# Kernel optimization log

Hardware: AMD Instinct MI355X
Metric: run time of the kernel (lower is better)

Reference implementation:

```python
import jax, jax.numpy as jnp
import numpy as np

B, S, D, H, L, OUT = 4, 1024, 1024, 16, 6, 512
HD = D // H
EPS = 1e-5


def _positional_encoding(seq, dim):
    pos = np.arange(seq, dtype=np.float32)[:, None]          # [S,1]
    i = np.arange(0, dim, 2, dtype=np.float32)[None, :]       # even indices
    div = np.power(10000.0, 2.0 * i / dim)                    # repo's (nonstandard) exponent
    pe = np.zeros((seq, dim), dtype=np.float32)
    pe[:, 0::2] = np.sin(pos / div)
    pe[:, 1::2] = np.cos(pos / div)
    return jnp.asarray(pe)[None]                               # [1,S,D]


def _causal_mask(seq):
    r = jnp.arange(seq)
    m = jnp.where(r[None, :] > r[:, None], jnp.float32(-jnp.inf), jnp.float32(0.0))
    return m[None, None]                                       # [1,1,S,S]


def setup_inputs() -> dict:
    key = jax.random.key(0)
    ks = jax.random.split(key, 10)
    sc = 0.02
    inp = {
        'x':      jax.random.normal(ks[0], (B, S, D), jnp.float32),
        'pe':     _positional_encoding(S, D),
        'mask':   _causal_mask(S),
        'ln1_g':  jnp.ones((L, D), jnp.float32),
        'ln1_b':  jnp.zeros((L, D), jnp.float32),
        'wq':     jax.random.normal(ks[1], (L, D, D), jnp.float32) * sc,
        'wk':     jax.random.normal(ks[2], (L, D, D), jnp.float32) * sc,
        'wv':     jax.random.normal(ks[3], (L, D, D), jnp.float32) * sc,
        'wo':     jax.random.normal(ks[4], (L, D, D), jnp.float32) * sc,
        'ln2_g':  jnp.ones((L, D), jnp.float32),
        'ln2_b':  jnp.zeros((L, D), jnp.float32),
        'wf':     jax.random.normal(ks[5], (L, D, D), jnp.float32) * sc,
        'lnf_g':  jnp.ones((D,), jnp.float32),
        'lnf_b':  jnp.zeros((D,), jnp.float32),
        'w_out':  jax.random.normal(ks[6], (OUT, D), jnp.float32) * sc,
    }
    return inp


def _layer_norm(x, g, b):
    mu = jnp.mean(x, axis=-1, keepdims=True)
    var = jnp.mean(jnp.square(x - mu), axis=-1, keepdims=True)
    return (x - mu) * jax.lax.rsqrt(var + EPS) * g + b


def _split_heads(x):
    b, s, d = x.shape
    return x.reshape(b, s, H, HD).transpose(0, 2, 1, 3)  # [B,H,S,HD]


def reference(x, pe, mask, ln1_g, ln1_b, wq, wk, wv, wo, ln2_g, ln2_b, wf, lnf_g, lnf_b, w_out):
    h = x + pe
    scale = 1.0 / jnp.sqrt(jnp.float32(HD))
    for l in range(wq.shape[0]):
        h_ = _layer_norm(h, ln1_g[l], ln1_b[l])
        q = _split_heads(jnp.einsum('bsd,ed->bse', h_, wq[l]))
        k = _split_heads(jnp.einsum('bsd,ed->bse', h_, wk[l]))
        v = _split_heads(jnp.einsum('bsd,ed->bse', h_, wv[l]))
        scores = jnp.einsum('bhqd,bhkd->bhqk', q, k) * scale + mask  # [B,H,S,S]
        probs = jax.nn.softmax(scores, axis=-1)
        attn = jnp.einsum('bhqk,bhkd->bhqd', probs, v)
        attn = attn.transpose(0, 2, 1, 3).reshape(h.shape)            # combine heads
        h = h + jnp.einsum('bsd,ed->bse', attn, wo[l])
        h_ = _layer_norm(h, ln2_g[l], ln2_b[l])
        h = h + jnp.einsum('bsd,ed->bse', h_, wf[l])                  # FFN = plain linear (no activation, as in source)
    h = _layer_norm(h, lnf_g, lnf_b)
    return jnp.einsum('bsd,od->bso', h, w_out)
```

## Files before the change

kernel.cpp:

```cpp
#include <hip/hip_runtime.h>
#include <hip/hip_bf16.h>
#include <stdint.h>

#define BATCH 4
#define SEQ   1024
#define DIM   1024
#define NH    16
#define HDIM  64
#define NLAYER 6
#define NOUT  512
#define NTOK  (BATCH*SEQ)
#define LOG2E 1.44269504088896f
#define NEG_BIG (-1e30f)
#define VTS   72

using bf16 = __hip_bfloat16;
typedef __attribute__((ext_vector_type(4))) float f32x4;
typedef __attribute__((ext_vector_type(8))) short bf16x8;

typedef __attribute__((address_space(1))) void as1_void;
typedef __attribute__((address_space(3))) void as3_void;

__device__ __forceinline__ float bf2f(short u) {
  union { unsigned int i; float f; } c;
  c.i = ((unsigned int)(unsigned short)u) << 16;
  return c.f;
}

__device__ __forceinline__ short f2bs(float f) {
  bf16 h = __float2bfloat16(f);
  return *(short*)&h;
}

__device__ __forceinline__ float exp_clamped(float x) {
  return exp2f(fmaxf(x, -100.f) * LOG2E);
}

__device__ __forceinline__ float loadf(const void* p, size_t i, bool f32) {
  return f32 ? ((const float*)p)[i] : __bfloat162float(((const bf16*)p)[i]);
}

__device__ __forceinline__ void g2l16(const void* g, void* l) {
  __builtin_amdgcn_global_load_lds((const as1_void*)g, (as3_void*)l, 16, 0, 0);
}

__global__ void sniff(const unsigned int* __restrict__ w, int* __restrict__ flag) {
  const int lane = threadIdx.x;
  const unsigned int word = w[lane];
  const int e2 = (word >> 7) & 0xFF;
  const bool bf16ish = (e2 >= 0x60) && (e2 <= 0x8F);
  const unsigned long long m = __ballot(bf16ish);
  if (lane == 0) *flag = (__popcll(m) >= 48) ? 0 : 1;
}

#define CV_BIG 786432
#define CV_TOT (5 * CV_BIG + 65536)

__global__ __launch_bounds__(256) void convert_all(
    const float* __restrict__ s0, const float* __restrict__ s1,
    const float* __restrict__ s2, const float* __restrict__ s3,
    const float* __restrict__ s4, const float* __restrict__ s5,
    bf16* __restrict__ d0, bf16* __restrict__ d1, bf16* __restrict__ d2,
    bf16* __restrict__ d3, bf16* __restrict__ d4, bf16* __restrict__ d5,
    const int* __restrict__ flag) {
  if (*flag == 0) return;
  for (size_t vi = (size_t)blockIdx.x * 256 + threadIdx.x; vi < CV_TOT;
       vi += (size_t)gridDim.x * 256) {
    const int t = (int)(vi / CV_BIG);
    const float* s; bf16* d;
    switch (t) {
      case 0: s = s0; d = d0; break;
      case 1: s = s1; d = d1; break;
      case 2: s = s2; d = d2; break;
      case 3: s = s3; d = d3; break;
      case 4: s = s4; d = d4; break;
      default: s = s5; d = d5; break;
    }
    const size_t off = (vi - (size_t)t * CV_BIG) * 8;
    const f32x4 a = *(const f32x4*)(s + off);
    const f32x4 b = *(const f32x4*)(s + off + 4);
    bf16x8 o;
    o[0] = f2bs(a[0]); o[1] = f2bs(a[1]); o[2] = f2bs(a[2]); o[3] = f2bs(a[3]);
    o[4] = f2bs(b[0]); o[5] = f2bs(b[1]); o[6] = f2bs(b[2]); o[7] = f2bs(b[3]);
    *(bf16x8*)(d + off) = o;
  }
}

template<int EPI>
__device__ __forceinline__ void gemm_body(const bf16* __restrict__ A,
                                          const bf16* __restrict__ W,
                                          void* __restrict__ C,
                                          const int* __restrict__ flag,
                                          int N, int m0, int n0) {
  __shared__ __align__(16) bf16 lA[128 * 32];
  __shared__ __align__(16) bf16 lB[128 * 32];
  const int tid  = threadIdx.x;
  const int wave = tid >> 6;
  const int lane = tid & 63;
  const int quad = lane >> 4;
  const int l16  = lane & 15;
  const int wm = (wave >> 1) * 64;
  const int wn = (wave & 1) * 64;
  const int K = DIM;

  const int r0 = tid >> 2;
  const int c0 = (tid & 3) * 8;
  const int r1 = (tid + 256) >> 2;

  bool f32out = false;
  if (EPI == 2) f32out = (*flag != 0);

  f32x4 acc[4][4];
#pragma unroll
  for (int i = 0; i < 4; ++i)
#pragma unroll
    for (int j = 0; j < 4; ++j) acc[i][j] = (f32x4){0.f, 0.f, 0.f, 0.f};

  for (int k0 = 0; k0 < K; k0 += 32) {
    __syncthreads();
    g2l16(A + (size_t)(m0 + r0) * K + k0 + c0, lA + 512 * wave);
    g2l16(A + (size_t)(m0 + r1) * K + k0 + c0, lA + 2048 + 512 * wave);
    g2l16(W + (size_t)(n0 + r0) * K + k0 + c0, lB + 512 * wave);
    g2l16(W + (size_t)(n0 + r1) * K + k0 + c0, lB + 2048 + 512 * wave);
    __builtin_amdgcn_s_waitcnt(0);
    __syncthreads();

    bf16x8 af[4], bfr[4];
#pragma unroll
    for (int i = 0; i < 4; ++i) {
      af[i]  = *(const bf16x8*)(lA + (wm + i * 16 + l16) * 32 + quad * 8);
      bfr[i] = *(const bf16x8*)(lB + (wn + i * 16 + l16) * 32 + quad * 8);
    }
#pragma unroll
    for (int i = 0; i < 4; ++i)
#pragma unroll
      for (int j = 0; j < 4; ++j)
        acc[i][j] = __builtin_amdgcn_mfma_f32_16x16x32_bf16(af[i], bfr[j], acc[i][j], 0, 0, 0);
  }

#pragma unroll
  for (int i = 0; i < 4; ++i) {
    const int rowb = m0 + wm + i * 16 + quad * 4;
#pragma unroll
    for (int j = 0; j < 4; ++j) {
      const int col = n0 + wn + j * 16 + l16;
#pragma unroll
      for (int r = 0; r < 4; ++r) {
        const size_t idx = (size_t)(rowb + r) * N + col;
        const float v = acc[i][j][r];
        if (EPI == 0) ((bf16*)C)[idx] = __float2bfloat16(v);
        else { if (f32out) ((float*)C)[idx] = v; else ((bf16*)C)[idx] = __float2bfloat16(v); }
      }
    }
  }
}

__global__ __launch_bounds__(256) void gemm_out(const bf16* __restrict__ A,
                                                const bf16* __restrict__ Wc,
                                                const bf16* __restrict__ Wo,
                                                void* __restrict__ C,
                                                const int* __restrict__ flag) {
  const bf16* W = (*flag != 0) ? Wc : Wo;
  gemm_body<2>(A, W, C, flag, NOUT, blockIdx.y * 128, blockIdx.x * 128);
}

__global__ __launch_bounds__(256) void gemm_qkv(const bf16* __restrict__ A,
                                                const bf16* __restrict__ cq,
                                                const bf16* __restrict__ ck,
                                                const bf16* __restrict__ cvv,
                                                const bf16* __restrict__ oq,
                                                const bf16* __restrict__ ok,
                                                const bf16* __restrict__ ov,
                                                bf16* __restrict__ q,
                                                bf16* __restrict__ k,
                                                bf16* __restrict__ v,
                                                const int* __restrict__ flag) {
  const int gx = blockIdx.x;
  const int sel = gx >> 3;
  const int n0 = (gx & 7) * 128;
  const bool f32 = (*flag != 0);
  const bf16* W = (sel == 0) ? (f32 ? cq : oq)
                 : (sel == 1) ? (f32 ? ck : ok)
                              : (f32 ? cvv : ov);
  bf16* C = (sel == 0) ? q : (sel == 1 ? k : v);
  gemm_body<0>(A, W, C, nullptr, DIM, blockIdx.y * 128, n0);
}

__device__ __forceinline__ void gemm64_body(const bf16* __restrict__ A,
                                            const bf16* __restrict__ W,
                                            float* __restrict__ C,
                                            int N, int m0, int n0) {
  __shared__ __align__(16) bf16 lA[64 * 32];
  __shared__ __align__(16) bf16 lB[128 * 32];
  const int tid  = threadIdx.x;
  const int wave = tid >> 6;
  const int lane = tid & 63;
  const int quad = lane >> 4;
  const int l16  = lane & 15;
  const int wm = (wave >> 1) * 32;
  const int wn = (wave & 1) * 64;
  const int K = DIM;

  const int r0 = tid >> 2;
  const int c0 = (tid & 3) * 8;
  const int r1 = (tid + 256) >> 2;

  f32x4 acc[2][4];
#pragma unroll
  for (int i = 0; i < 2; ++i)
#pragma unroll
    for (int j = 0; j < 4; ++j) acc[i][j] = (f32x4){0.f, 0.f, 0.f, 0.f};

  for (int k0 = 0; k0 < K; k0 += 32) {
    __syncthreads();
    g2l16(A + (size_t)(m0 + r0) * K + k0 + c0, lA + 512 * wave);
    g2l16(W + (size_t)(n0 + r0) * K + k0 + c0, lB + 512 * wave);
    g2l16(W + (size_t)(n0 + r1) * K + k0 + c0, lB + 2048 + 512 * wave);
    __builtin_amdgcn_s_waitcnt(0);
    __syncthreads();

    bf16x8 af[2], bfr[4];
#pragma unroll
    for (int i = 0; i < 2; ++i)
      af[i]  = *(const bf16x8*)(lA + (wm + i * 16 + l16) * 32 + quad * 8);
#pragma unroll
    for (int j = 0; j < 4; ++j)
      bfr[j] = *(const bf16x8*)(lB + (wn + j * 16 + l16) * 32 + quad * 8);
#pragma unroll
    for (int i = 0; i < 2; ++i)
#pragma unroll
      for (int j = 0; j < 4; ++j)
        acc[i][j] = __builtin_amdgcn_mfma_f32_16x16x32_bf16(af[i], bfr[j], acc[i][j], 0, 0, 0);
  }

#pragma unroll
  for (int i = 0; i < 2; ++i) {
    const int rowb = m0 + wm + i * 16 + quad * 4;
#pragma unroll
    for (int j = 0; j < 4; ++j) {
      const int col = n0 + wn + j * 16 + l16;
#pragma unroll
      for (int r = 0; r < 4; ++r)
        C[(size_t)(rowb + r) * N + col] += acc[i][j][r];
    }
  }
}

__global__ __launch_bounds__(256) void gemm_add(const bf16* __restrict__ A,
                                                const bf16* __restrict__ Wc,
                                                const bf16* __restrict__ Wo,
                                                const int* __restrict__ flag,
                                                float* __restrict__ C) {
  const bf16* W = (*flag != 0) ? Wc : Wo;
  gemm64_body(A, W, C, DIM, blockIdx.y * 64, blockIdx.x * 128);
}

__global__ __launch_bounds__(256) void add_pe(const void* __restrict__ x,
                                              const void* __restrict__ pe,
                                              float* __restrict__ h,
                                              const int* __restrict__ flag) {
  const bool f32 = (*flag != 0);
  const size_t i = (size_t)blockIdx.x * 256 + threadIdx.x;
  h[i] = loadf(x, i, f32) + loadf(pe, i & (SEQ * DIM - 1), f32);
}

__global__ __launch_bounds__(256) void layernorm(const float* __restrict__ x,
                                                 const void* __restrict__ g,
                                                 const void* __restrict__ b,
                                                 int loff,
                                                 bf16* __restrict__ y,
                                                 const int* __restrict__ flag) {
  const bool f32 = (*flag != 0);
  const int row = blockIdx.x;
  const int tid = threadIdx.x;
  const int wave = tid >> 6;
  const float* xr = x + (size_t)row * DIM;
  __shared__ float red[8];

  float v[4];
  float s = 0.f;
#pragma unroll
  for (int i = 0; i < 4; ++i) { v[i] = xr[tid + 256 * i]; s += v[i]; }
#pragma unroll
  for (int off = 32; off >= 1; off >>= 1) s += __shfl_xor(s, off);
  if ((tid & 63) == 0) red[wave] = s;
  __syncthreads();
  const float mu = (red[0] + red[1] + red[2] + red[3]) * (1.f / DIM);

  float vs = 0.f;
#pragma unroll
  for (int i = 0; i < 4; ++i) { const float d = v[i] - mu; vs += d * d; }
#pragma unroll
  for (int off = 32; off >= 1; off >>= 1) vs += __shfl_xor(vs, off);
  if ((tid & 63) == 0) red[4 + wave] = vs;
  __syncthreads();
  const float var = (red[4] + red[5] + red[6] + red[7]) * (1.f / DIM);
  const float rs = rsqrtf(var + 1e-5f);

#pragma unroll
  for (int i = 0; i < 4; ++i) {
    const int d = tid + 256 * i;
    const float gv = loadf(g, (size_t)loff + d, f32);
    const float bv = loadf(b, (size_t)loff + d, f32);
    y[(size_t)row * DIM + d] = __float2bfloat16((v[i] - mu) * rs * gv + bv);
  }
}

__global__ __launch_bounds__(256, 2) void attn_flash(const bf16* __restrict__ q,
                                                     const bf16* __restrict__ k,
                                                     const bf16* __restrict__ v,
                                                     bf16* __restrict__ o) {
  __shared__ __align__(16) short lK[64 * 64];
  __shared__ __align__(16) short lVT[64 * VTS];
  __shared__ __align__(16) short lP[4 * 16 * VTS];

  const int idx = blockIdx.x;
  const int qt = (SEQ / 64 - 1) - (idx >> 6);
  const int bh = idx & 63;
  const int hh = bh & (NH - 1);
  const int bb = bh >> 4;
  const int q0 = qt * 64;

  const int tid = threadIdx.x;
  const int wave = tid >> 6;
  const int lane = tid & 63;
  const int quad = lane >> 4;
  const int l16 = lane & 15;

  const size_t base = (size_t)bb * SEQ * DIM + hh * HDIM;
  const int qlo = q0 + wave * 16;

  bf16x8 qf[2];
  {
    const bf16* qr = q + base + (size_t)(qlo + l16) * DIM;
#pragma unroll
    for (int kc = 0; kc < 2; ++kc) {
      bf16x8 t = *(const bf16x8*)(qr + kc * 32 + quad * 8);
      bf16x8 sq;
#pragma unroll
      for (int e = 0; e < 8; ++e) sq[e] = f2bs(bf2f(t[e]) * 0.125f);
      qf[kc] = sq;
    }
  }

  float l_acc[4] = {0.f, 0.f, 0.f, 0.f};
  f32x4 oacc[4];
#pragma unroll
  for (int nb = 0; nb < 4; ++nb) oacc[nb] = (f32x4){0.f, 0.f, 0.f, 0.f};

  short* lPw = lP + wave * 16 * VTS;
  const int nt = qt + 1;

  for (int t = 0; t < nt; ++t) {
    const int kbase = t * 64;
    __syncthreads();

    {
      const int r8 = lane >> 3;
      const int cc = (lane & 7) ^ r8;
#pragma unroll
      for (int c = 0; c < 2; ++c) {
        const int row = wave * 16 + c * 8 + r8;
        g2l16(k + base + (size_t)(kbase + row) * DIM + cc * 8,
              lK + (wave * 16 + c * 8) * 64);
      }
    }

    bf16x8 vch[2];
#pragma unroll
    for (int c2 = 0; c2 < 2; ++c2) {
      const int cid = tid + c2 * 256;
      const int kk = cid >> 3;
      const int d0 = (cid & 7) * 8;
      vch[c2] = *(const bf16x8*)(v + base + (size_t)(kbase + kk) * DIM + d0);
    }
#pragma unroll
    for (int c2 = 0; c2 < 2; ++c2) {
      const int cid = tid + c2 * 256;
      const int kk = cid >> 3;
      const int d0 = (cid & 7) * 8;
#pragma unroll
      for (int e = 0; e < 8; ++e) {
        const int d = d0 + e;
        const int kks = kk ^ (((d >> 3) & 7) << 3);
        lVT[d * VTS + kks] = vch[c2][e];
      }
    }
    __builtin_amdgcn_s_waitcnt(0);
    __syncthreads();

    f32x4 s[4];
#pragma unroll
    for (int nb = 0; nb < 4; ++nb) {
      f32x4 acc = (f32x4){0.f, 0.f, 0.f, 0.f};
      const int n = nb * 16 + l16;
#pragma unroll
      for (int kc = 0; kc < 2; ++kc) {
        const int cidx = (kc * 4 + quad) ^ (n & 7);
        bf16x8 kf = *(const bf16x8*)(lK + n * 64 + cidx * 8);
        acc = __builtin_amdgcn_mfma_f32_16x16x32_bf16(qf[kc], kf, acc, 0, 0, 0);
      }
      s[nb] = acc;
    }

    if (kbase + 63 > qlo) {
#pragma unroll
      for (int nb = 0; nb < 4; ++nb) {
        const int j = kbase + nb * 16 + l16;
#pragma unroll
        for (int r = 0; r < 4; ++r)
          if (j > qlo + quad * 4 + r) s[nb][r] = NEG_BIG;
      }
    }

#pragma unroll
    for (int nb = 0; nb < 4; ++nb) {
#pragma unroll
      for (int r = 0; r < 4; ++r) {
        const float p = exp_clamped(s[nb][r]);
        l_acc[r] += p;
        lPw[(quad * 4 + r) * VTS + nb * 16 + l16] = f2bs(p);
      }
    }

    __builtin_amdgcn_s_waitcnt(0);
    bf16x8 pf[2];
#pragma unroll
    for (int kc = 0; kc < 2; ++kc)
      pf[kc] = *(const bf16x8*)(lPw + l16 * VTS + kc * 32 + quad * 8);

#pragma unroll
    for (int nb = 0; nb < 4; ++nb) {
      const int n = nb * 16 + l16;
      const int swz = ((n >> 3) & 7) << 3;
#pragma unroll
      for (int kc = 0; kc < 2; ++kc) {
        const int kchunk = (kc * 32 + quad * 8) ^ swz;
        bf16x8 vf = *(const bf16x8*)(lVT + n * VTS + kchunk);
        oacc[nb] = __builtin_amdgcn_mfma_f32_16x16x32_bf16(pf[kc], vf, oacc[nb], 0, 0, 0);
      }
    }
  }

  float linv[4];
#pragma unroll
  for (int r = 0; r < 4; ++r) {
    float ts = l_acc[r];
#pragma unroll
    for (int off = 8; off >= 1; off >>= 1) ts += __shfl_xor(ts, off);
    linv[r] = 1.f / ts;
  }
#pragma unroll
  for (int nb = 0; nb < 4; ++nb)
#pragma unroll
    for (int r = 0; r < 4; ++r) {
      const int qrow = q0 + wave * 16 + quad * 4 + r;
      o[base + (size_t)qrow * DIM + nb * 16 + l16] =
          __float2bfloat16(oacc[nb][r] * linv[r]);
    }
}

extern "C" void kernel_launch(void* const* d_in, const int* in_sizes, int n_in,
                              void* d_out, int out_size, void* d_ws, size_t ws_size,
                              hipStream_t stream) {
  const void* x    = d_in[0];
  const void* pe   = d_in[1];
  const void* ln1g = d_in[3];
  const void* ln1b = d_in[4];
  const void* wq   = d_in[5];
  const void* wk   = d_in[6];
  const void* wv   = d_in[7];
  const void* wo   = d_in[8];
  const void* ln2g = d_in[9];
  const void* ln2b = d_in[10];
  const void* wf   = d_in[11];
  const void* lnfg = d_in[12];
  const void* lnfb = d_in[13];
  const void* wout = d_in[14];

  const size_t MB = 1u << 20;
  char* ws = (char*)d_ws;
  int*  flag = (int*)ws;
  bf16* wqc  = (bf16*)(ws + 1 * MB);
  bf16* wkc  = (bf16*)(ws + 13 * MB);
  bf16* wvc  = (bf16*)(ws + 25 * MB);
  bf16* woc  = (bf16*)(ws + 37 * MB);
  bf16* wfc  = (bf16*)(ws + 49 * MB);
  bf16* woutc= (bf16*)(ws + 61 * MB);
  float* h   = (float*)(ws + 62 * MB);
  bf16* hn   = (bf16*)(ws + 78 * MB);
  bf16* qb   = (bf16*)(ws + 86 * MB);
  bf16* kb   = (bf16*)(ws + 94 * MB);
  bf16* vb   = (bf16*)(ws + 102 * MB);
  bf16* ab   = hn;

  sniff<<<1, 64, 0, stream>>>((const unsigned int*)wq, flag);

  convert_all<<<2048, 256, 0, stream>>>(
      (const float*)wq, (const float*)wk, (const float*)wv,
      (const float*)wo, (const float*)wf, (const float*)wout,
      wqc, wkc, wvc, woc, wfc, woutc, flag);

  add_pe<<<NTOK * DIM / 256, 256, 0, stream>>>(x, pe, h, flag);

  for (int l = 0; l < NLAYER; ++l) {
    const size_t woff = (size_t)l << 20;
    const int poff = l * DIM;
    layernorm<<<NTOK, 256, 0, stream>>>(h, ln1g, ln1b, poff, hn, flag);
    gemm_qkv<<<dim3(24, 32), 256, 0, stream>>>(
        hn, wqc + woff, wkc + woff, wvc + woff,
        (const bf16*)wq + woff, (const bf16*)wk + woff, (const bf16*)wv + woff,
        qb, kb, vb, flag);
    attn_flash<<<dim3(BATCH * NH * (SEQ / 64)), 256, 0, stream>>>(qb, kb, vb, ab);
    gemm_add<<<dim3(8, 64), 256, 0, stream>>>(ab, woc + woff,
                                              (const bf16*)wo + woff, flag, h);
    layernorm<<<NTOK, 256, 0, stream>>>(h, ln2g, ln2b, poff, hn, flag);
    gemm_add<<<dim3(8, 64), 256, 0, stream>>>(hn, wfc + woff,
                                              (const bf16*)wf + woff, flag, h);
  }

  layernorm<<<NTOK, 256, 0, stream>>>(h, lnfg, lnfb, 0, hn, flag);
  gemm_out<<<dim3(4, 32), 256, 0, stream>>>(hn, woutc, (const bf16*)wout,
                                            d_out, flag);
}
```

Before: 966.4 us.

## Remap GEMM and attention block IDs for XCD-aware L2 locality; restructure weight conversion

Block indices for the QKV, projection, output GEMMs and flash attention are remapped so that blocks dispatched round-robin across the 8 XCDs (obid & 7) handle contiguous tiles. Tiles sharing weight columns or the same batch-head then land on one XCD and can reuse its L2. The weight conversion kernel also drops its grid-stride loop with a division for a fixed block-to-tensor mapping, with four vector loads per thread to raise memory-level parallelism. The cost is hardcoded grid sizes tied to the exact problem dimensions.

```diff
diff --git a/kernel.cpp b/kernel.cpp
--- a/kernel.cpp
+++ b/kernel.cpp
@@ -53,9 +53,6 @@
   if (lane == 0) *flag = (__popcll(m) >= 48) ? 0 : 1;
 }
 
-#define CV_BIG 786432
-#define CV_TOT (5 * CV_BIG + 65536)
-
 __global__ __launch_bounds__(256) void convert_all(
     const float* __restrict__ s0, const float* __restrict__ s1,
     const float* __restrict__ s2, const float* __restrict__ s3,
@@ -64,25 +61,27 @@
     bf16* __restrict__ d3, bf16* __restrict__ d4, bf16* __restrict__ d5,
     const int* __restrict__ flag) {
   if (*flag == 0) return;
-  for (size_t vi = (size_t)blockIdx.x * 256 + threadIdx.x; vi < CV_TOT;
-       vi += (size_t)gridDim.x * 256) {
-    const int t = (int)(vi / CV_BIG);
-    const float* s; bf16* d;
-    switch (t) {
-      case 0: s = s0; d = d0; break;
-      case 1: s = s1; d = d1; break;
-      case 2: s = s2; d = d2; break;
-      case 3: s = s3; d = d3; break;
-      case 4: s = s4; d = d4; break;
-      default: s = s5; d = d5; break;
-    }
-    const size_t off = (vi - (size_t)t * CV_BIG) * 8;
-    const f32x4 a = *(const f32x4*)(s + off);
-    const f32x4 b = *(const f32x4*)(s + off + 4);
+  int b = blockIdx.x;
+  const float* s; bf16* d;
+  if      (b <  768) { s = s0; d = d0; }
+  else if (b < 1536) { s = s1; d = d1; b -= 768; }
+  else if (b < 2304) { s = s2; d = d2; b -= 1536; }
+  else if (b < 3072) { s = s3; d = d3; b -= 2304; }
+  else if (b < 3840) { s = s4; d = d4; b -= 3072; }
+  else               { s = s5; d = d5; b -= 3840; }
+  const size_t e0 = ((size_t)b * 1024 + threadIdx.x) * 8;
+  f32x4 a[4], c[4];
+#pragma unroll
+  for (int i = 0; i < 4; ++i) {
+    a[i] = *(const f32x4*)(s + e0 + i * 2048);
+    c[i] = *(const f32x4*)(s + e0 + i * 2048 + 4);
+  }
+#pragma unroll
+  for (int i = 0; i < 4; ++i) {
     bf16x8 o;
-    o[0] = f2bs(a[0]); o[1] = f2bs(a[1]); o[2] = f2bs(a[2]); o[3] = f2bs(a[3]);
-    o[4] = f2bs(b[0]); o[5] = f2bs(b[1]); o[6] = f2bs(b[2]); o[7] = f2bs(b[3]);
-    *(bf16x8*)(d + off) = o;
+    o[0] = f2bs(a[i][0]); o[1] = f2bs(a[i][1]); o[2] = f2bs(a[i][2]); o[3] = f2bs(a[i][3]);
+    o[4] = f2bs(c[i][0]); o[5] = f2bs(c[i][1]); o[6] = f2bs(c[i][2]); o[7] = f2bs(c[i][3]);
+    *(bf16x8*)(d + e0 + i * 2048) = o;
   }
 }
 
@@ -160,8 +159,12 @@
                                                 const bf16* __restrict__ Wo,
                                                 void* __restrict__ C,
                                                 const int* __restrict__ flag) {
+  const int obid = blockIdx.x;
+  const int wid = (obid & 7) * 16 + (obid >> 3);
+  const int m0 = (wid & 31) * 128;
+  const int n0 = (wid >> 5) * 128;
   const bf16* W = (*flag != 0) ? Wc : Wo;
-  gemm_body<2>(A, W, C, flag, NOUT, blockIdx.y * 128, blockIdx.x * 128);
+  gemm_body<2>(A, W, C, flag, NOUT, m0, n0);
 }
 
 __global__ __launch_bounds__(256) void gemm_qkv(const bf16* __restrict__ A,
@@ -175,15 +178,18 @@
                                                 bf16* __restrict__ k,
                                                 bf16* __restrict__ v,
                                                 const int* __restrict__ flag) {
-  const int gx = blockIdx.x;
-  const int sel = gx >> 3;
-  const int n0 = (gx & 7) * 128;
+  const int obid = blockIdx.x;
+  const int wid = (obid & 7) * 96 + (obid >> 3);
+  const int m0   = (wid & 31) * 128;
+  const int rest = wid >> 5;
+  const int sel  = rest >> 3;
+  const int n0   = (rest & 7) * 128;
   const bool f32 = (*flag != 0);
   const bf16* W = (sel == 0) ? (f32 ? cq : oq)
                  : (sel == 1) ? (f32 ? ck : ok)
                               : (f32 ? cvv : ov);
   bf16* C = (sel == 0) ? q : (sel == 1 ? k : v);
-  gemm_body<0>(A, W, C, nullptr, DIM, blockIdx.y * 128, n0);
+  gemm_body<0>(A, W, C, nullptr, DIM, m0, n0);
 }
 
 __device__ __forceinline__ void gemm64_body(const bf16* __restrict__ A,
@@ -251,8 +257,12 @@
                                                 const bf16* __restrict__ Wo,
                                                 const int* __restrict__ flag,
                                                 float* __restrict__ C) {
+  const int obid = blockIdx.x;
+  const int wid = (obid & 7) * 64 + (obid >> 3);
+  const int m0 = (wid & 63) * 64;
+  const int n0 = (wid >> 6) * 128;
   const bf16* W = (*flag != 0) ? Wc : Wo;
-  gemm64_body(A, W, C, DIM, blockIdx.y * 64, blockIdx.x * 128);
+  gemm64_body(A, W, C, DIM, m0, n0);
 }
 
 __global__ __launch_bounds__(256) void add_pe(const void* __restrict__ x,
@@ -314,9 +324,10 @@
   __shared__ __align__(16) short lVT[64 * VTS];
   __shared__ __align__(16) short lP[4 * 16 * VTS];
 
-  const int idx = blockIdx.x;
-  const int qt = (SEQ / 64 - 1) - (idx >> 6);
-  const int bh = idx & 63;
+  const int obid = blockIdx.x;
+  const int wid = (obid & 7) * 128 + (obid >> 3);
+  const int bh = wid >> 4;
+  const int qt = 15 - (wid & 15);
   const int hh = bh & (NH - 1);
   const int bb = bh >> 4;
   const int q0 = qt * 64;
@@ -496,7 +507,7 @@
 
   sniff<<<1, 64, 0, stream>>>((const unsigned int*)wq, flag);
 
-  convert_all<<<2048, 256, 0, stream>>>(
+  convert_all<<<3904, 256, 0, stream>>>(
       (const float*)wq, (const float*)wk, (const float*)wv,
       (const float*)wo, (const float*)wf, (const float*)wout,
       wqc, wkc, wvc, woc, wfc, woutc, flag);
@@ -507,19 +518,19 @@
     const size_t woff = (size_t)l << 20;
     const int poff = l * DIM;
     layernorm<<<NTOK, 256, 0, stream>>>(h, ln1g, ln1b, poff, hn, flag);
-    gemm_qkv<<<dim3(24, 32), 256, 0, stream>>>(
+    gemm_qkv<<<dim3(768), 256, 0, stream>>>(
         hn, wqc + woff, wkc + woff, wvc + woff,
         (const bf16*)wq + woff, (const bf16*)wk + woff, (const bf16*)wv + woff,
         qb, kb, vb, flag);
     attn_flash<<<dim3(BATCH * NH * (SEQ / 64)), 256, 0, stream>>>(qb, kb, vb, ab);
-    gemm_add<<<dim3(8, 64), 256, 0, stream>>>(ab, woc + woff,
-                                              (const bf16*)wo + woff, flag, h);
+    gemm_add<<<dim3(512), 256, 0, stream>>>(ab, woc + woff,
+                                            (const bf16*)wo + woff, flag, h);
     layernorm<<<NTOK, 256, 0, stream>>>(h, ln2g, ln2b, poff, hn, flag);
-    gemm_add<<<dim3(8, 64), 256, 0, stream>>>(hn, wfc + woff,
-                                              (const bf16*)wf + woff, flag, h);
+    gemm_add<<<dim3(512), 256, 0, stream>>>(hn, wfc + woff,
+                                            (const bf16*)wf + woff, flag, h);
   }
 
   layernorm<<<NTOK, 256, 0, stream>>>(h, lnfg, lnfb, 0, hn, flag);
-  gemm_out<<<dim3(4, 32), 256, 0, stream>>>(hn, woutc, (const bf16*)wout,
-                                            d_out, flag);
-}
+  gemm_out<<<dim3(128), 256, 0, stream>>>(hn, woutc, (const bf16*)wout,
+                                          d_out, flag);
+}
```

After: 1.042 ms. 1.08x slower.
